# Kernel optimization log

Hardware: AMD Instinct MI355X
Metric: run time of the kernel (lower is better)

## Reference

```python
import jax, jax.numpy as jnp
import numpy as np


def _maxpool2x2(t):
    # t: [B, C, H, W] -> [B, C, H//2, W//2]
    B, C, H, W = t.shape
    return t.reshape(B, C, H // 2, 2, W // 2, 2).max(axis=(3, 5))


def setup_inputs() -> dict:
    key = jax.random.key(0)
    ks = jax.random.split(key, 6)
    ch = 64
    B, H, W = 16, 64, 64
    x = jax.random.normal(ks[0], (B, ch, H, W), dtype=jnp.float32)
    # 1x1 conv weights (spectral-norm wrapper just rescales weights; use unit-scale weights)
    w_theta = jax.random.normal(ks[1], (ch // 8, ch), dtype=jnp.float32) * 0.05
    w_phi = jax.random.normal(ks[2], (ch // 8, ch), dtype=jnp.float32) * 0.05
    w_g = jax.random.normal(ks[3], (ch // 2, ch), dtype=jnp.float32) * 0.05
    w_o = jax.random.normal(ks[4], (ch, ch // 2), dtype=jnp.float32) * 0.05
    gamma = jnp.float32(0.5)  # nonzero so attention branch contributes
    return {"x": x, "w_theta": w_theta, "w_phi": w_phi, "w_g": w_g, "w_o": w_o, "gamma": gamma}


def reference(x, w_theta, w_phi, w_g, w_o, gamma):
    B, C, H, W = x.shape
    N = H * W
    # 1x1 convs are channel contractions
    theta = jnp.einsum('oc,bchw->bohw', w_theta, x).reshape(B, -1, N)          # [B, C/8, N]
    phi = _maxpool2x2(jnp.einsum('oc,bchw->bohw', w_phi, x)).reshape(B, -1, N // 4)  # [B, C/8, N/4]
    g = _maxpool2x2(jnp.einsum('oc,bchw->bohw', w_g, x)).reshape(B, -1, N // 4)      # [B, C/2, N/4]
    # attention: no scaling (faithful to source)
    scores = jnp.einsum('bdn,bdm->bnm', theta, phi)       # [B, N, N/4]
    beta = jax.nn.softmax(scores, axis=-1)
    o = jnp.einsum('bdm,bnm->bdn', g, beta)               # [B, C/2, N]
    o = o.reshape(B, C // 2, H, W)
    o = jnp.einsum('oc,bchw->bohw', w_o, o)               # [B, C, H, W]
    return gamma * o + x
```

## Files before the change

### kernel.cpp

```cpp
#include <hip/hip_runtime.h>
#include <hip/hip_bf16.h>

#define BB 16
#define CC 64
#define NN 4096
#define MM 1024

typedef unsigned short u16;
typedef unsigned int u32;
typedef __attribute__((ext_vector_type(8))) short bf16x8;
typedef __attribute__((ext_vector_type(4))) float f32x4;

__device__ inline u16 f2bf(float f) {
    union { float f; u32 u; } v; v.f = f;
    return (u16)((v.u + 0x7FFFu + ((v.u >> 16) & 1u)) >> 16);
}
__device__ inline bf16x8 ld_bf16x8(const u16* p) {
    union { uint4 u; bf16x8 b; } c; c.u = *(const uint4*)p; return c.b;
}
__device__ inline bf16x8 ld2_bf16x8(const u16* p0, const u16* p1) {
    union { uint2 u[2]; bf16x8 b; } c;
    c.u[0] = *(const uint2*)p0;
    c.u[1] = *(const uint2*)p1;
    return c.b;
}
__device__ inline u32 cvt_pk_bf16(float lo, float hi) {
    __hip_bfloat162 h = __float22bfloat162_rn(make_float2(lo, hi));
    return *(u32*)&h;
}


__global__ __launch_bounds__(256) void prep_kernel(
    const float* __restrict__ x, const float* __restrict__ w_theta,
    const float* __restrict__ w_phi, const float* __restrict__ w_g,
    u16* __restrict__ theta_b, u16* __restrict__ phi_b, u16* __restrict__ gT_b)
{
    const int t = threadIdx.x, w = t >> 6, lane = t & 63;
    const int m16 = lane & 15, quad = lane >> 4;
    const int b = blockIdx.y, bx = blockIdx.x;
    const int nbase = bx * 256;

    bf16x8 A[3][2];
    {
        const float* row0 = (m16 < 8) ? (w_theta + m16 * 64) : (w_phi + (m16 - 8) * 64);
        const float* rows[3] = { row0, w_g + m16 * 64, w_g + (16 + m16) * 64 };
        #pragma unroll
        for (int f = 0; f < 3; ++f) {
            #pragma unroll
            for (int kc = 0; kc < 2; ++kc) {
                const float* p = rows[f] + kc * 32 + quad * 8;
                const float4 f0 = *(const float4*)p;
                const float4 f1 = *(const float4*)(p + 4);
                union { u32 d[4]; bf16x8 v; } a;
                a.d[0] = cvt_pk_bf16(f0.x, f0.y);
                a.d[1] = cvt_pk_bf16(f0.z, f0.w);
                a.d[2] = cvt_pk_bf16(f1.x, f1.y);
                a.d[3] = cvt_pk_bf16(f1.z, f1.w);
                A[f][kc] = a.v;
            }
        }
    }

    const float* xb = x + (size_t)b * CC * NN;
    const f32x4 zero4 = {0.f, 0.f, 0.f, 0.f};
    f32x4 acc[4][3];
    #pragma unroll
    for (int r = 0; r < 4; ++r)
        #pragma unroll
        for (int f = 0; f < 3; ++f) acc[r][f] = zero4;

    #pragma unroll
    for (int r = 0; r < 4; ++r) {
        const int px = nbase + r * 64 + w * 16 + m16;
        #pragma unroll
        for (int kc = 0; kc < 2; ++kc) {
            float xv[8];
            #pragma unroll
            for (int j = 0; j < 8; ++j)
                xv[j] = xb[(size_t)(kc * 32 + quad * 8 + j) * NN + px];
            union { u32 d[4]; bf16x8 v; } bxf;
            bxf.d[0] = cvt_pk_bf16(xv[0], xv[1]);
            bxf.d[1] = cvt_pk_bf16(xv[2], xv[3]);
            bxf.d[2] = cvt_pk_bf16(xv[4], xv[5]);
            bxf.d[3] = cvt_pk_bf16(xv[6], xv[7]);
            #pragma unroll
            for (int f = 0; f < 3; ++f)
                acc[r][f] = __builtin_amdgcn_mfma_f32_16x16x32_bf16(A[f][kc], bxf.v, acc[r][f], 0, 0, 0);
        }
    }

    if (quad < 2) {
        #pragma unroll
        for (int r = 0; r < 4; ++r) {
            const int px = nbase + r * 64 + w * 16 + m16;
            uint2 v;
            v.x = cvt_pk_bf16(acc[r][0][0], acc[r][0][1]);
            v.y = cvt_pk_bf16(acc[r][0][2], acc[r][0][3]);
            *(uint2*)(theta_b + ((size_t)b * NN + px) * 8 + quad * 4) = v;
        }
    }

    float pv[2][3][4];
    #pragma unroll
    for (int f = 0; f < 3; ++f)
        #pragma unroll
        for (int rr = 0; rr < 4; ++rr) {
            float h0 = acc[0][f][rr]; h0 = fmaxf(h0, __shfl_xor(h0, 1, 64));
            float h1 = acc[1][f][rr]; h1 = fmaxf(h1, __shfl_xor(h1, 1, 64));
            float h2 = acc[2][f][rr]; h2 = fmaxf(h2, __shfl_xor(h2, 1, 64));
            float h3 = acc[3][f][rr]; h3 = fmaxf(h3, __shfl_xor(h3, 1, 64));
            pv[0][f][rr] = fmaxf(h0, h1);
            pv[1][f][rr] = fmaxf(h2, h3);
        }

    if ((m16 & 1) == 0) {
        const int pcol = w * 8 + (m16 >> 1);
        #pragma unroll
        for (int rp = 0; rp < 2; ++rp) {
            const int m = (2 * bx + rp) * 32 + pcol;
            if (quad >= 2) {
                uint2 v;
                v.x = cvt_pk_bf16(pv[rp][0][0], pv[rp][0][1]);
                v.y = cvt_pk_bf16(pv[rp][0][2], pv[rp][0][3]);
                *(uint2*)(phi_b + ((size_t)b * MM + m) * 8 + (quad - 2) * 4) = v;
            }
            #pragma unroll
            for (int f = 1; f < 3; ++f)
                #pragma unroll
                for (int rr = 0; rr < 4; ++rr) {
                    const int d = (f - 1) * 16 + quad * 4 + rr;
                    gT_b[(size_t)b * 32 * MM + (size_t)d * MM + m] = f2bf(pv[rp][f][rr]);
                }
        }
    }
}

__global__ __launch_bounds__(256, 4) void attn_out_kernel(
    const u16* __restrict__ theta_b, const u16* __restrict__ phi_b,
    const u16* __restrict__ gT_b, const float* __restrict__ w_o,
    const float* __restrict__ x, const float* __restrict__ gamma_p,
    float* __restrict__ out)
{
    __shared__ u16 phis[1024 * 8];
    __shared__ u16 gs[32 * 264];
    __shared__ u16 oS[64 * 40];

    const int t = threadIdx.x, w = t >> 6, lane = t & 63;
    const int m16 = lane & 15, quad = lane >> 4;
    const int b = blockIdx.y, qbase = blockIdx.x * 64;

    const u16* phg = phi_b + (size_t)b * MM * 8;
    const u16* gtg = gT_b + (size_t)b * 32 * MM;

    #pragma unroll
    for (int i = 0; i < 4; ++i)
        ((uint4*)phis)[i * 256 + t] = ((const uint4*)phg)[i * 256 + t];

    bf16x8 thB = {0, 0, 0, 0, 0, 0, 0, 0};
    if (quad == 0)
        thB = ld_bf16x8(theta_b + ((size_t)b * NN + qbase + w * 16 + m16) * 8);

    bf16x8 woA[4];
    #pragma unroll
    for (int cf = 0; cf < 4; ++cf) {
        const float* wp = w_o + (cf * 16 + m16) * 32 + quad * 8;
        const float4 f0 = *(const float4*)wp;
        const float4 f1 = *(const float4*)(wp + 4);
        union { u32 d[4]; bf16x8 v; } a;
        a.d[0] = cvt_pk_bf16(f0.x, f0.y);
        a.d[1] = cvt_pk_bf16(f0.z, f0.w);
        a.d[2] = cvt_pk_bf16(f1.x, f1.y);
        a.d[3] = cvt_pk_bf16(f1.z, f1.w);
        woA[cf] = a.v;
    }

    bf16x8 onesA;
    #pragma unroll
    for (int i = 0; i < 8; ++i) onesA[i] = (short)0x3F80;

    const f32x4 zero4 = {0.f, 0.f, 0.f, 0.f};
    f32x4 oT0 = zero4, oT1 = zero4, lacc = zero4;

    uint4 r[4];
    #pragma unroll
    for (int i = 0; i < 4; ++i) {
        const int f = i * 256 + t, d = f >> 5, ku = f & 31;
        r[i] = *(const uint4*)(gtg + (size_t)d * MM + ku * 8);
    }

    for (int c = 0; c < 4; ++c) {
        __syncthreads();
        #pragma unroll
        for (int i = 0; i < 4; ++i) {
            const int f = i * 256 + t, d = f >> 5, ku = f & 31;
            *(uint4*)(gs + d * 264 + ku * 8) = r[i];
        }
        __syncthreads();
        if (c < 3) {
            #pragma unroll
            for (int i = 0; i < 4; ++i) {
                const int f = i * 256 + t, d = f >> 5, ku = f & 31;
                r[i] = *(const uint4*)(gtg + (size_t)d * MM + (c + 1) * 256 + ku * 8);
            }
        }

        #pragma unroll
        for (int kblk = 0; kblk < 8; ++kblk) {
            const int kb = c * 256 + kblk * 32;
            bf16x8 phA0 = {0, 0, 0, 0, 0, 0, 0, 0};
            bf16x8 phA1 = {0, 0, 0, 0, 0, 0, 0, 0};
            if (quad == 0) {
                phA0 = ld_bf16x8(phis + (size_t)(kb + m16) * 8);
                phA1 = ld_bf16x8(phis + (size_t)(kb + 16 + m16) * 8);
            }
            const f32x4 Sa = __builtin_amdgcn_mfma_f32_16x16x32_bf16(phA0, thB, zero4, 0, 0, 0);
            const f32x4 Sb = __builtin_amdgcn_mfma_f32_16x16x32_bf16(phA1, thB, zero4, 0, 0, 0);

            union { u32 d[4]; bf16x8 v; } pb;
            pb.d[0] = cvt_pk_bf16(__expf(Sa[0]), __expf(Sa[1]));
            pb.d[1] = cvt_pk_bf16(__expf(Sa[2]), __expf(Sa[3]));
            pb.d[2] = cvt_pk_bf16(__expf(Sb[0]), __expf(Sb[1]));
            pb.d[3] = cvt_pk_bf16(__expf(Sb[2]), __expf(Sb[3]));

            const u16* g0p = gs + m16 * 264 + kblk * 32 + quad * 4;
            const u16* g1p = gs + (16 + m16) * 264 + kblk * 32 + quad * 4;
            const bf16x8 gA0 = ld2_bf16x8(g0p, g0p + 16);
            const bf16x8 gA1 = ld2_bf16x8(g1p, g1p + 16);

            oT0  = __builtin_amdgcn_mfma_f32_16x16x32_bf16(gA0, pb.v, oT0, 0, 0, 0);
            oT1  = __builtin_amdgcn_mfma_f32_16x16x32_bf16(gA1, pb.v, oT1, 0, 0, 0);
            lacc = __builtin_amdgcn_mfma_f32_16x16x32_bf16(onesA, pb.v, lacc, 0, 0, 0);
        }
    }

    const float inv = 1.0f / lacc[0];
    u16* orow = oS + (w * 16 + m16) * 40;
    {
        uint2 a, b2;
        a.x  = cvt_pk_bf16(oT0[0] * inv, oT0[1] * inv);
        a.y  = cvt_pk_bf16(oT0[2] * inv, oT0[3] * inv);
        b2.x = cvt_pk_bf16(oT1[0] * inv, oT1[1] * inv);
        b2.y = cvt_pk_bf16(oT1[2] * inv, oT1[3] * inv);
        *(uint2*)(orow + quad * 4) = a;
        *(uint2*)(orow + 16 + quad * 4) = b2;
    }
    __syncthreads();

    const bf16x8 oB = ld_bf16x8(oS + (w * 16 + m16) * 40 + quad * 8);
    const float gamma = *gamma_p;
    #pragma unroll
    for (int cf = 0; cf < 4; ++cf) {
        const f32x4 D = __builtin_amdgcn_mfma_f32_16x16x32_bf16(woA[cf], oB, zero4, 0, 0, 0);
        #pragma unroll
        for (int rr = 0; rr < 4; ++rr) {
            const int cch = cf * 16 + quad * 4 + rr;
            const size_t adr = ((size_t)b * CC + cch) * NN + qbase + w * 16 + m16;
            out[adr] = gamma * D[rr] + x[adr];
        }
    }
}

extern "C" void kernel_launch(void* const* d_in, const int* in_sizes, int n_in,
                              void* d_out, int out_size, void* d_ws, size_t ws_size,
                              hipStream_t stream) {
    const float* x       = (const float*)d_in[0];
    const float* w_theta = (const float*)d_in[1];
    const float* w_phi   = (const float*)d_in[2];
    const float* w_g     = (const float*)d_in[3];
    const float* w_o     = (const float*)d_in[4];
    const float* gamma   = (const float*)d_in[5];

    u16* theta_b = (u16*)d_ws;
    u16* phi_b   = theta_b + 524288;
    u16* gT_b    = phi_b + 131072;
    float* out   = (float*)d_out;

    prep_kernel<<<dim3(16, 16), 256, 0, stream>>>(x, w_theta, w_phi, w_g,
                                                  theta_b, phi_b, gT_b);
    attn_out_kernel<<<dim3(64, 16), 256, 0, stream>>>(theta_b, phi_b, gT_b,
                                                      w_o, x, gamma, out);
}
```

Before: 113.7 us.

## Double queries per attention block, fold log2e into theta, shrink prep tiles

The attention kernel now has each wave handle two 16-query tiles, so every phi/g fragment loaded from LDS is reused twice and the g staging cost is spread over 128 queries per block. The grid halves to 512 blocks and launch bounds drop to 2 waves-per-SIMD to make room for the extra registers. Theta is pre-scaled by log2(e) so the softmax uses exp2f in place of __expf. The prep kernel moves to 128-pixel tiles, doubling its block count for better occupancy. The risks are fewer attention blocks and higher register pressure, which could hurt latency hiding.

```diff
diff --git a/kernel.cpp b/kernel.cpp
--- a/kernel.cpp
+++ b/kernel.cpp
@@ -5,6 +5,7 @@
 #define CC 64
 #define NN 4096
 #define MM 1024
+#define LOG2E 1.4426950408889634f
 
 typedef unsigned short u16;
 typedef unsigned int u32;
@@ -38,7 +39,7 @@
     const int t = threadIdx.x, w = t >> 6, lane = t & 63;
     const int m16 = lane & 15, quad = lane >> 4;
     const int b = blockIdx.y, bx = blockIdx.x;
-    const int nbase = bx * 256;
+    const int nbase = bx * 128;
 
     bf16x8 A[3][2];
     {
@@ -63,14 +64,14 @@
 
     const float* xb = x + (size_t)b * CC * NN;
     const f32x4 zero4 = {0.f, 0.f, 0.f, 0.f};
-    f32x4 acc[4][3];
-    #pragma unroll
-    for (int r = 0; r < 4; ++r)
+    f32x4 acc[2][3];
+    #pragma unroll
+    for (int r = 0; r < 2; ++r)
         #pragma unroll
         for (int f = 0; f < 3; ++f) acc[r][f] = zero4;
 
     #pragma unroll
-    for (int r = 0; r < 4; ++r) {
+    for (int r = 0; r < 2; ++r) {
         const int px = nbase + r * 64 + w * 16 + m16;
         #pragma unroll
         for (int kc = 0; kc < 2; ++kc) {
@@ -91,51 +92,45 @@
 
     if (quad < 2) {
         #pragma unroll
-        for (int r = 0; r < 4; ++r) {
+        for (int r = 0; r < 2; ++r) {
             const int px = nbase + r * 64 + w * 16 + m16;
             uint2 v;
-            v.x = cvt_pk_bf16(acc[r][0][0], acc[r][0][1]);
-            v.y = cvt_pk_bf16(acc[r][0][2], acc[r][0][3]);
+            v.x = cvt_pk_bf16(acc[r][0][0] * LOG2E, acc[r][0][1] * LOG2E);
+            v.y = cvt_pk_bf16(acc[r][0][2] * LOG2E, acc[r][0][3] * LOG2E);
             *(uint2*)(theta_b + ((size_t)b * NN + px) * 8 + quad * 4) = v;
         }
     }
 
-    float pv[2][3][4];
+    float pv[3][4];
     #pragma unroll
     for (int f = 0; f < 3; ++f)
         #pragma unroll
         for (int rr = 0; rr < 4; ++rr) {
             float h0 = acc[0][f][rr]; h0 = fmaxf(h0, __shfl_xor(h0, 1, 64));
             float h1 = acc[1][f][rr]; h1 = fmaxf(h1, __shfl_xor(h1, 1, 64));
-            float h2 = acc[2][f][rr]; h2 = fmaxf(h2, __shfl_xor(h2, 1, 64));
-            float h3 = acc[3][f][rr]; h3 = fmaxf(h3, __shfl_xor(h3, 1, 64));
-            pv[0][f][rr] = fmaxf(h0, h1);
-            pv[1][f][rr] = fmaxf(h2, h3);
+            pv[f][rr] = fmaxf(h0, h1);
         }
 
     if ((m16 & 1) == 0) {
         const int pcol = w * 8 + (m16 >> 1);
-        #pragma unroll
-        for (int rp = 0; rp < 2; ++rp) {
-            const int m = (2 * bx + rp) * 32 + pcol;
-            if (quad >= 2) {
-                uint2 v;
-                v.x = cvt_pk_bf16(pv[rp][0][0], pv[rp][0][1]);
-                v.y = cvt_pk_bf16(pv[rp][0][2], pv[rp][0][3]);
-                *(uint2*)(phi_b + ((size_t)b * MM + m) * 8 + (quad - 2) * 4) = v;
-            }
-            #pragma unroll
-            for (int f = 1; f < 3; ++f)
-                #pragma unroll
-                for (int rr = 0; rr < 4; ++rr) {
-                    const int d = (f - 1) * 16 + quad * 4 + rr;
-                    gT_b[(size_t)b * 32 * MM + (size_t)d * MM + m] = f2bf(pv[rp][f][rr]);
-                }
-        }
-    }
-}
-
-__global__ __launch_bounds__(256, 4) void attn_out_kernel(
+        const int m = bx * 32 + pcol;
+        if (quad >= 2) {
+            uint2 v;
+            v.x = cvt_pk_bf16(pv[0][0], pv[0][1]);
+            v.y = cvt_pk_bf16(pv[0][2], pv[0][3]);
+            *(uint2*)(phi_b + ((size_t)b * MM + m) * 8 + (quad - 2) * 4) = v;
+        }
+        #pragma unroll
+        for (int f = 1; f < 3; ++f)
+            #pragma unroll
+            for (int rr = 0; rr < 4; ++rr) {
+                const int d = (f - 1) * 16 + quad * 4 + rr;
+                gT_b[(size_t)b * 32 * MM + (size_t)d * MM + m] = f2bf(pv[f][rr]);
+            }
+    }
+}
+
+__global__ __launch_bounds__(256, 2) void attn_out_kernel(
     const u16* __restrict__ theta_b, const u16* __restrict__ phi_b,
     const u16* __restrict__ gT_b, const float* __restrict__ w_o,
     const float* __restrict__ x, const float* __restrict__ gamma_p,
@@ -143,11 +138,11 @@
 {
     __shared__ u16 phis[1024 * 8];
     __shared__ u16 gs[32 * 264];
-    __shared__ u16 oS[64 * 40];
+    __shared__ u16 oS[128 * 40];
 
     const int t = threadIdx.x, w = t >> 6, lane = t & 63;
     const int m16 = lane & 15, quad = lane >> 4;
-    const int b = blockIdx.y, qbase = blockIdx.x * 64;
+    const int b = blockIdx.y, qbase = blockIdx.x * 128;
 
     const u16* phg = phi_b + (size_t)b * MM * 8;
     const u16* gtg = gT_b + (size_t)b * 32 * MM;
@@ -156,9 +151,12 @@
     for (int i = 0; i < 4; ++i)
         ((uint4*)phis)[i * 256 + t] = ((const uint4*)phg)[i * 256 + t];
 
-    bf16x8 thB = {0, 0, 0, 0, 0, 0, 0, 0};
-    if (quad == 0)
-        thB = ld_bf16x8(theta_b + ((size_t)b * NN + qbase + w * 16 + m16) * 8);
+    bf16x8 thB[2] = {{0,0,0,0,0,0,0,0}, {0,0,0,0,0,0,0,0}};
+    if (quad == 0) {
+        #pragma unroll
+        for (int u = 0; u < 2; ++u)
+            thB[u] = ld_bf16x8(theta_b + ((size_t)b * NN + qbase + w * 32 + u * 16 + m16) * 8);
+    }
 
     bf16x8 woA[4];
     #pragma unroll
@@ -179,7 +177,7 @@
     for (int i = 0; i < 8; ++i) onesA[i] = (short)0x3F80;
 
     const f32x4 zero4 = {0.f, 0.f, 0.f, 0.f};
-    f32x4 oT0 = zero4, oT1 = zero4, lacc = zero4;
+    f32x4 oT0[2] = {zero4, zero4}, oT1[2] = {zero4, zero4}, lacc[2] = {zero4, zero4};
 
     uint4 r[4];
     #pragma unroll
@@ -213,49 +211,56 @@
                 phA0 = ld_bf16x8(phis + (size_t)(kb + m16) * 8);
                 phA1 = ld_bf16x8(phis + (size_t)(kb + 16 + m16) * 8);
             }
-            const f32x4 Sa = __builtin_amdgcn_mfma_f32_16x16x32_bf16(phA0, thB, zero4, 0, 0, 0);
-            const f32x4 Sb = __builtin_amdgcn_mfma_f32_16x16x32_bf16(phA1, thB, zero4, 0, 0, 0);
-
-            union { u32 d[4]; bf16x8 v; } pb;
-            pb.d[0] = cvt_pk_bf16(__expf(Sa[0]), __expf(Sa[1]));
-            pb.d[1] = cvt_pk_bf16(__expf(Sa[2]), __expf(Sa[3]));
-            pb.d[2] = cvt_pk_bf16(__expf(Sb[0]), __expf(Sb[1]));
-            pb.d[3] = cvt_pk_bf16(__expf(Sb[2]), __expf(Sb[3]));
-
             const u16* g0p = gs + m16 * 264 + kblk * 32 + quad * 4;
             const u16* g1p = gs + (16 + m16) * 264 + kblk * 32 + quad * 4;
             const bf16x8 gA0 = ld2_bf16x8(g0p, g0p + 16);
             const bf16x8 gA1 = ld2_bf16x8(g1p, g1p + 16);
 
-            oT0  = __builtin_amdgcn_mfma_f32_16x16x32_bf16(gA0, pb.v, oT0, 0, 0, 0);
-            oT1  = __builtin_amdgcn_mfma_f32_16x16x32_bf16(gA1, pb.v, oT1, 0, 0, 0);
-            lacc = __builtin_amdgcn_mfma_f32_16x16x32_bf16(onesA, pb.v, lacc, 0, 0, 0);
-        }
-    }
-
-    const float inv = 1.0f / lacc[0];
-    u16* orow = oS + (w * 16 + m16) * 40;
-    {
+            #pragma unroll
+            for (int u = 0; u < 2; ++u) {
+                const f32x4 Sa = __builtin_amdgcn_mfma_f32_16x16x32_bf16(phA0, thB[u], zero4, 0, 0, 0);
+                const f32x4 Sb = __builtin_amdgcn_mfma_f32_16x16x32_bf16(phA1, thB[u], zero4, 0, 0, 0);
+
+                union { u32 d[4]; bf16x8 v; } pb;
+                pb.d[0] = cvt_pk_bf16(exp2f(Sa[0]), exp2f(Sa[1]));
+                pb.d[1] = cvt_pk_bf16(exp2f(Sa[2]), exp2f(Sa[3]));
+                pb.d[2] = cvt_pk_bf16(exp2f(Sb[0]), exp2f(Sb[1]));
+                pb.d[3] = cvt_pk_bf16(exp2f(Sb[2]), exp2f(Sb[3]));
+
+                oT0[u]  = __builtin_amdgcn_mfma_f32_16x16x32_bf16(gA0, pb.v, oT0[u], 0, 0, 0);
+                oT1[u]  = __builtin_amdgcn_mfma_f32_16x16x32_bf16(gA1, pb.v, oT1[u], 0, 0, 0);
+                lacc[u] = __builtin_amdgcn_mfma_f32_16x16x32_bf16(onesA, pb.v, lacc[u], 0, 0, 0);
+            }
+        }
+    }
+
+    #pragma unroll
+    for (int u = 0; u < 2; ++u) {
+        const float inv = 1.0f / lacc[u][0];
+        u16* orow = oS + (size_t)(w * 32 + u * 16 + m16) * 40;
         uint2 a, b2;
-        a.x  = cvt_pk_bf16(oT0[0] * inv, oT0[1] * inv);
-        a.y  = cvt_pk_bf16(oT0[2] * inv, oT0[3] * inv);
-        b2.x = cvt_pk_bf16(oT1[0] * inv, oT1[1] * inv);
-        b2.y = cvt_pk_bf16(oT1[2] * inv, oT1[3] * inv);
+        a.x  = cvt_pk_bf16(oT0[u][0] * inv, oT0[u][1] * inv);
+        a.y  = cvt_pk_bf16(oT0[u][2] * inv, oT0[u][3] * inv);
+        b2.x = cvt_pk_bf16(oT1[u][0] * inv, oT1[u][1] * inv);
+        b2.y = cvt_pk_bf16(oT1[u][2] * inv, oT1[u][3] * inv);
         *(uint2*)(orow + quad * 4) = a;
         *(uint2*)(orow + 16 + quad * 4) = b2;
     }
     __syncthreads();
 
-    const bf16x8 oB = ld_bf16x8(oS + (w * 16 + m16) * 40 + quad * 8);
     const float gamma = *gamma_p;
     #pragma unroll
-    for (int cf = 0; cf < 4; ++cf) {
-        const f32x4 D = __builtin_amdgcn_mfma_f32_16x16x32_bf16(woA[cf], oB, zero4, 0, 0, 0);
-        #pragma unroll
-        for (int rr = 0; rr < 4; ++rr) {
-            const int cch = cf * 16 + quad * 4 + rr;
-            const size_t adr = ((size_t)b * CC + cch) * NN + qbase + w * 16 + m16;
-            out[adr] = gamma * D[rr] + x[adr];
+    for (int u = 0; u < 2; ++u) {
+        const bf16x8 oB = ld_bf16x8(oS + (size_t)(w * 32 + u * 16 + m16) * 40 + quad * 8);
+        #pragma unroll
+        for (int cf = 0; cf < 4; ++cf) {
+            const f32x4 D = __builtin_amdgcn_mfma_f32_16x16x32_bf16(woA[cf], oB, zero4, 0, 0, 0);
+            #pragma unroll
+            for (int rr = 0; rr < 4; ++rr) {
+                const int cch = cf * 16 + quad * 4 + rr;
+                const size_t adr = ((size_t)b * CC + cch) * NN + qbase + w * 32 + u * 16 + m16;
+                out[adr] = gamma * D[rr] + x[adr];
+            }
         }
     }
 }
@@ -275,8 +280,8 @@
     u16* gT_b    = phi_b + 131072;
     float* out   = (float*)d_out;
 
-    prep_kernel<<<dim3(16, 16), 256, 0, stream>>>(x, w_theta, w_phi, w_g,
+    prep_kernel<<<dim3(32, 16), 256, 0, stream>>>(x, w_theta, w_phi, w_g,
                                                   theta_b, phi_b, gT_b);
-    attn_out_kernel<<<dim3(64, 16), 256, 0, stream>>>(theta_b, phi_b, gT_b,
+    attn_out_kernel<<<dim3(32, 16), 256, 0, stream>>>(theta_b, phi_b, gT_b,
                                                       w_o, x, gamma, out);
 }
```

Measured after the change: 115.0 us. About the same (+1.1%).

## Read phi/g directly from global in attention, fold log2e into theta, halve prep tiles

Applied to the files above, without the earlier changes.

The attention kernel no longer stages phi and g through shared memory with barriers. Each wave now loads its MFMA operands straight from global memory, relying on L2/L1 caching, and runs a single unrolled loop over all key blocks. Theta is pre-scaled by log2(e) so the softmax can use exp2f instead of __expf. The prep kernel processes 128 pixels per block instead of 256, doubling its grid for more parallelism. The barrier before reading oS was removed; each wave reads only its own rows, so this relies on wave-local ordering of LDS writes and reads. The trade-off is more uncoalesced, redundant global loads in exchange for fewer barriers and lower LDS usage.

```diff
diff --git a/kernel.cpp b/kernel.cpp
--- a/kernel.cpp
+++ b/kernel.cpp
@@ -5,6 +5,7 @@
 #define CC 64
 #define NN 4096
 #define MM 1024
+#define LOG2E 1.4426950408889634f
 
 typedef unsigned short u16;
 typedef unsigned int u32;
@@ -38,14 +39,14 @@
     const int t = threadIdx.x, w = t >> 6, lane = t & 63;
     const int m16 = lane & 15, quad = lane >> 4;
     const int b = blockIdx.y, bx = blockIdx.x;
-    const int nbase = bx * 256;
+    const int nbase = bx * 128;
 
     bf16x8 A[3][2];
     {
         const float* row0 = (m16 < 8) ? (w_theta + m16 * 64) : (w_phi + (m16 - 8) * 64);
         const float* rows[3] = { row0, w_g + m16 * 64, w_g + (16 + m16) * 64 };
         #pragma unroll
-        for (int f = 0; f < 3; ++f) {
+        for (int f = 0; f < 3; ++f)
             #pragma unroll
             for (int kc = 0; kc < 2; ++kc) {
                 const float* p = rows[f] + kc * 32 + quad * 8;
@@ -58,26 +59,25 @@
                 a.d[3] = cvt_pk_bf16(f1.z, f1.w);
                 A[f][kc] = a.v;
             }
-        }
     }
 
     const float* xb = x + (size_t)b * CC * NN;
     const f32x4 zero4 = {0.f, 0.f, 0.f, 0.f};
-    f32x4 acc[4][3];
-    #pragma unroll
-    for (int r = 0; r < 4; ++r)
+    f32x4 acc[2][3];
+    #pragma unroll
+    for (int r = 0; r < 2; ++r)
         #pragma unroll
         for (int f = 0; f < 3; ++f) acc[r][f] = zero4;
 
     #pragma unroll
-    for (int r = 0; r < 4; ++r) {
+    for (int r = 0; r < 2; ++r) {
         const int px = nbase + r * 64 + w * 16 + m16;
         #pragma unroll
         for (int kc = 0; kc < 2; ++kc) {
             float xv[8];
             #pragma unroll
-            for (int j = 0; j < 8; ++j)
-                xv[j] = xb[(size_t)(kc * 32 + quad * 8 + j) * NN + px];
+            for (int jj = 0; jj < 8; ++jj)
+                xv[jj] = xb[(size_t)(kc * 32 + quad * 8 + jj) * NN + px];
             union { u32 d[4]; bf16x8 v; } bxf;
             bxf.d[0] = cvt_pk_bf16(xv[0], xv[1]);
             bxf.d[1] = cvt_pk_bf16(xv[2], xv[3]);
@@ -91,47 +91,41 @@
 
     if (quad < 2) {
         #pragma unroll
-        for (int r = 0; r < 4; ++r) {
+        for (int r = 0; r < 2; ++r) {
             const int px = nbase + r * 64 + w * 16 + m16;
             uint2 v;
-            v.x = cvt_pk_bf16(acc[r][0][0], acc[r][0][1]);
-            v.y = cvt_pk_bf16(acc[r][0][2], acc[r][0][3]);
+            v.x = cvt_pk_bf16(acc[r][0][0] * LOG2E, acc[r][0][1] * LOG2E);
+            v.y = cvt_pk_bf16(acc[r][0][2] * LOG2E, acc[r][0][3] * LOG2E);
             *(uint2*)(theta_b + ((size_t)b * NN + px) * 8 + quad * 4) = v;
         }
     }
 
-    float pv[2][3][4];
+    float pv[3][4];
     #pragma unroll
     for (int f = 0; f < 3; ++f)
         #pragma unroll
         for (int rr = 0; rr < 4; ++rr) {
             float h0 = acc[0][f][rr]; h0 = fmaxf(h0, __shfl_xor(h0, 1, 64));
             float h1 = acc[1][f][rr]; h1 = fmaxf(h1, __shfl_xor(h1, 1, 64));
-            float h2 = acc[2][f][rr]; h2 = fmaxf(h2, __shfl_xor(h2, 1, 64));
-            float h3 = acc[3][f][rr]; h3 = fmaxf(h3, __shfl_xor(h3, 1, 64));
-            pv[0][f][rr] = fmaxf(h0, h1);
-            pv[1][f][rr] = fmaxf(h2, h3);
+            pv[f][rr] = fmaxf(h0, h1);
         }
 
     if ((m16 & 1) == 0) {
         const int pcol = w * 8 + (m16 >> 1);
-        #pragma unroll
-        for (int rp = 0; rp < 2; ++rp) {
-            const int m = (2 * bx + rp) * 32 + pcol;
-            if (quad >= 2) {
-                uint2 v;
-                v.x = cvt_pk_bf16(pv[rp][0][0], pv[rp][0][1]);
-                v.y = cvt_pk_bf16(pv[rp][0][2], pv[rp][0][3]);
-                *(uint2*)(phi_b + ((size_t)b * MM + m) * 8 + (quad - 2) * 4) = v;
+        const int m = bx * 32 + pcol;
+        if (quad >= 2) {
+            uint2 v;
+            v.x = cvt_pk_bf16(pv[0][0], pv[0][1]);
+            v.y = cvt_pk_bf16(pv[0][2], pv[0][3]);
+            *(uint2*)(phi_b + ((size_t)b * MM + m) * 8 + (quad - 2) * 4) = v;
+        }
+        #pragma unroll
+        for (int f = 1; f < 3; ++f)
+            #pragma unroll
+            for (int rr = 0; rr < 4; ++rr) {
+                const int d = (f - 1) * 16 + quad * 4 + rr;
+                gT_b[(size_t)b * 32 * MM + (size_t)d * MM + m] = f2bf(pv[f][rr]);
             }
-            #pragma unroll
-            for (int f = 1; f < 3; ++f)
-                #pragma unroll
-                for (int rr = 0; rr < 4; ++rr) {
-                    const int d = (f - 1) * 16 + quad * 4 + rr;
-                    gT_b[(size_t)b * 32 * MM + (size_t)d * MM + m] = f2bf(pv[rp][f][rr]);
-                }
-        }
     }
 }
 
@@ -141,8 +135,6 @@
     const float* __restrict__ x, const float* __restrict__ gamma_p,
     float* __restrict__ out)
 {
-    __shared__ u16 phis[1024 * 8];
-    __shared__ u16 gs[32 * 264];
     __shared__ u16 oS[64 * 40];
 
     const int t = threadIdx.x, w = t >> 6, lane = t & 63;
@@ -151,10 +143,6 @@
 
     const u16* phg = phi_b + (size_t)b * MM * 8;
     const u16* gtg = gT_b + (size_t)b * 32 * MM;
-
-    #pragma unroll
-    for (int i = 0; i < 4; ++i)
-        ((uint4*)phis)[i * 256 + t] = ((const uint4*)phg)[i * 256 + t];
 
     bf16x8 thB = {0, 0, 0, 0, 0, 0, 0, 0};
     if (quad == 0)
@@ -173,7 +161,6 @@
         a.d[3] = cvt_pk_bf16(f1.z, f1.w);
         woA[cf] = a.v;
     }
-
     bf16x8 onesA;
     #pragma unroll
     for (int i = 0; i < 8; ++i) onesA[i] = (short)0x3F80;
@@ -181,60 +168,34 @@
     const f32x4 zero4 = {0.f, 0.f, 0.f, 0.f};
     f32x4 oT0 = zero4, oT1 = zero4, lacc = zero4;
 
-    uint4 r[4];
-    #pragma unroll
-    for (int i = 0; i < 4; ++i) {
-        const int f = i * 256 + t, d = f >> 5, ku = f & 31;
-        r[i] = *(const uint4*)(gtg + (size_t)d * MM + ku * 8);
-    }
-
-    for (int c = 0; c < 4; ++c) {
-        __syncthreads();
-        #pragma unroll
-        for (int i = 0; i < 4; ++i) {
-            const int f = i * 256 + t, d = f >> 5, ku = f & 31;
-            *(uint4*)(gs + d * 264 + ku * 8) = r[i];
-        }
-        __syncthreads();
-        if (c < 3) {
-            #pragma unroll
-            for (int i = 0; i < 4; ++i) {
-                const int f = i * 256 + t, d = f >> 5, ku = f & 31;
-                r[i] = *(const uint4*)(gtg + (size_t)d * MM + (c + 1) * 256 + ku * 8);
-            }
-        }
-
-        #pragma unroll
-        for (int kblk = 0; kblk < 8; ++kblk) {
-            const int kb = c * 256 + kblk * 32;
-            bf16x8 phA0 = {0, 0, 0, 0, 0, 0, 0, 0};
-            bf16x8 phA1 = {0, 0, 0, 0, 0, 0, 0, 0};
-            if (quad == 0) {
-                phA0 = ld_bf16x8(phis + (size_t)(kb + m16) * 8);
-                phA1 = ld_bf16x8(phis + (size_t)(kb + 16 + m16) * 8);
-            }
-            const f32x4 Sa = __builtin_amdgcn_mfma_f32_16x16x32_bf16(phA0, thB, zero4, 0, 0, 0);
-            const f32x4 Sb = __builtin_amdgcn_mfma_f32_16x16x32_bf16(phA1, thB, zero4, 0, 0, 0);
-
-            union { u32 d[4]; bf16x8 v; } pb;
-            pb.d[0] = cvt_pk_bf16(__expf(Sa[0]), __expf(Sa[1]));
-            pb.d[1] = cvt_pk_bf16(__expf(Sa[2]), __expf(Sa[3]));
-            pb.d[2] = cvt_pk_bf16(__expf(Sb[0]), __expf(Sb[1]));
-            pb.d[3] = cvt_pk_bf16(__expf(Sb[2]), __expf(Sb[3]));
-
-            const u16* g0p = gs + m16 * 264 + kblk * 32 + quad * 4;
-            const u16* g1p = gs + (16 + m16) * 264 + kblk * 32 + quad * 4;
-            const bf16x8 gA0 = ld2_bf16x8(g0p, g0p + 16);
-            const bf16x8 gA1 = ld2_bf16x8(g1p, g1p + 16);
-
-            oT0  = __builtin_amdgcn_mfma_f32_16x16x32_bf16(gA0, pb.v, oT0, 0, 0, 0);
-            oT1  = __builtin_amdgcn_mfma_f32_16x16x32_bf16(gA1, pb.v, oT1, 0, 0, 0);
-            lacc = __builtin_amdgcn_mfma_f32_16x16x32_bf16(onesA, pb.v, lacc, 0, 0, 0);
-        }
+    #pragma unroll 4
+    for (int kblk = 0; kblk < 32; ++kblk) {
+        const int kb = kblk * 32;
+
+        const bf16x8 phA0 = ld_bf16x8(phg + (size_t)(kb + m16) * 8);
+        const bf16x8 phA1 = ld_bf16x8(phg + (size_t)(kb + 16 + m16) * 8);
+
+        const u16* g0p = gtg + (size_t)m16 * MM + kb + quad * 4;
+        const u16* g1p = gtg + (size_t)(16 + m16) * MM + kb + quad * 4;
+        const bf16x8 gA0 = ld2_bf16x8(g0p, g0p + 16);
+        const bf16x8 gA1 = ld2_bf16x8(g1p, g1p + 16);
+
+        const f32x4 Sa = __builtin_amdgcn_mfma_f32_16x16x32_bf16(phA0, thB, zero4, 0, 0, 0);
+        const f32x4 Sb = __builtin_amdgcn_mfma_f32_16x16x32_bf16(phA1, thB, zero4, 0, 0, 0);
+
+        union { u32 d[4]; bf16x8 v; } pb;
+        pb.d[0] = cvt_pk_bf16(exp2f(Sa[0]), exp2f(Sa[1]));
+        pb.d[1] = cvt_pk_bf16(exp2f(Sa[2]), exp2f(Sa[3]));
+        pb.d[2] = cvt_pk_bf16(exp2f(Sb[0]), exp2f(Sb[1]));
+        pb.d[3] = cvt_pk_bf16(exp2f(Sb[2]), exp2f(Sb[3]));
+
+        oT0  = __builtin_amdgcn_mfma_f32_16x16x32_bf16(gA0, pb.v, oT0, 0, 0, 0);
+        oT1  = __builtin_amdgcn_mfma_f32_16x16x32_bf16(gA1, pb.v, oT1, 0, 0, 0);
+        lacc = __builtin_amdgcn_mfma_f32_16x16x32_bf16(onesA, pb.v, lacc, 0, 0, 0);
     }
 
     const float inv = 1.0f / lacc[0];
-    u16* orow = oS + (w * 16 + m16) * 40;
+    u16* orow = oS + (size_t)(w * 16 + m16) * 40;
     {
         uint2 a, b2;
         a.x  = cvt_pk_bf16(oT0[0] * inv, oT0[1] * inv);
@@ -244,9 +205,8 @@
         *(uint2*)(orow + quad * 4) = a;
         *(uint2*)(orow + 16 + quad * 4) = b2;
     }
-    __syncthreads();
-
-    const bf16x8 oB = ld_bf16x8(oS + (w * 16 + m16) * 40 + quad * 8);
+
+    const bf16x8 oB = ld_bf16x8(oS + (size_t)(w * 16 + m16) * 40 + quad * 8);
     const float gamma = *gamma_p;
     #pragma unroll
     for (int cf = 0; cf < 4; ++cf) {
@@ -275,7 +235,7 @@
     u16* gT_b    = phi_b + 131072;
     float* out   = (float*)d_out;
 
-    prep_kernel<<<dim3(16, 16), 256, 0, stream>>>(x, w_theta, w_phi, w_g,
+    prep_kernel<<<dim3(32, 16), 256, 0, stream>>>(x, w_theta, w_phi, w_g,
                                                   theta_b, phi_b, gT_b);
     attn_out_kernel<<<dim3(64, 16), 256, 0, stream>>>(theta_b, phi_b, gT_b,
                                                       w_o, x, gamma, out);
```

Measured after the change: 149.8 us. 1.32x slower.
